# Kernel optimization log

Hardware: AMD Instinct MI355X
Metric: run time of the kernel (lower is better)

## Reference

```python
import jax, jax.numpy as jnp
import numpy as np

N_NODES = 50000
N_EDGES = 500000
D_IN, D_HID = 128, 256


def _add_self_loops(edge_index, n):
    loop = jnp.arange(n, dtype=edge_index.dtype)
    src = jnp.concatenate([edge_index[0], loop])
    dst = jnp.concatenate([edge_index[1], loop])
    return src, dst


def _gcn_layer(x, W, b, src, dst, dinv_sqrt, n):
    # x: [N, d_in] -> h: [N, d_out]
    h = x @ W
    # symmetric normalization D^{-1/2} (A+I) D^{-1/2}
    norm = dinv_sqrt[src] * dinv_sqrt[dst]          # [E+N]
    msg = h[src] * norm[:, None]                    # gather + scale
    agg = jax.ops.segment_sum(msg, dst, num_segments=n)  # scatter-add
    return agg + b


def setup_inputs() -> dict:
    key = jax.random.key(0)
    ks = jax.random.split(key, 8)
    x = jax.random.normal(ks[0], (N_NODES, D_IN), dtype=jnp.float32)
    edge_index = jax.random.randint(ks[1], (2, N_EDGES), 0, N_NODES, dtype=jnp.int64 if jax.config.read('jax_enable_x64') else jnp.int32)
    s = lambda fan_in: 1.0 / np.sqrt(fan_in)
    W1 = jax.random.uniform(ks[2], (D_IN, D_HID), jnp.float32, -s(D_IN), s(D_IN))
    b1 = jnp.zeros((D_HID,), jnp.float32)
    W2 = jax.random.uniform(ks[3], (D_HID, D_HID), jnp.float32, -s(D_HID), s(D_HID))
    b2 = jnp.zeros((D_HID,), jnp.float32)
    W3 = jax.random.uniform(ks[4], (D_HID, D_HID), jnp.float32, -s(D_HID), s(D_HID))
    b3 = jnp.zeros((D_HID,), jnp.float32)
    return {"x": x, "edge_index": edge_index, "W1": W1, "b1": b1,
            "W2": W2, "b2": b2, "W3": W3, "b3": b3}


def reference(x, edge_index, W1, b1, W2, b2, W3, b3):
    n = x.shape[0]
    src, dst = _add_self_loops(edge_index, n)
    # degree includes self loops (edge weight 1), as in torch_geometric GCNConv
    deg = jax.ops.segment_sum(jnp.ones_like(dst, dtype=x.dtype), dst, num_segments=n)
    dinv_sqrt = jnp.where(deg > 0, jax.lax.rsqrt(jnp.maximum(deg, 1e-12)), 0.0)
    h = jax.nn.relu(_gcn_layer(x, W1, b1, src, dst, dinv_sqrt, n))
    h = jax.nn.relu(_gcn_layer(h, W2, b2, src, dst, dinv_sqrt, n))
    h = _gcn_layer(h, W3, b3, src, dst, dinv_sqrt, n)
    return h
```

## Files before the change

### kernel.cpp

```cpp
#include <hip/hip_runtime.h>

#define NNODES 50000
#define NEDGES 500000
#define DIN 128
#define DHID 256
#define MPAD 50048
#define NI4 12500
#define NSB 49

typedef unsigned short u16;
typedef __attribute__((ext_vector_type(8))) _Float16 half8;
typedef __attribute__((ext_vector_type(4))) float f32x4;

__device__ __forceinline__ u16 f2h(float f) {
  union { _Float16 h; u16 u; } v; v.h = (_Float16)f; return v.u;
}
__device__ __forceinline__ float h2f(unsigned int u) {
  union { _Float16 h; u16 u; } v; v.u = (u16)u; return (float)v.h;
}

#define GLDS16(g, l) __builtin_amdgcn_global_load_lds( \
    (const __attribute__((address_space(1))) void*)(g), \
    (__attribute__((address_space(3))) void*)(l), 16, 0, 0)

__global__ void k_zero_i32(int* __restrict__ p, int n) {
  int i = blockIdx.x * blockDim.x + threadIdx.x;
  if (i < n) p[i] = 0;
}

__global__ void k_hist(const int* __restrict__ dst, int* __restrict__ deg, int e) {
  int i = blockIdx.x * blockDim.x + threadIdx.x;
  if (i < e) atomicAdd(&deg[dst[i]], 1);
}

__global__ __launch_bounds__(256) void k_blocksum(const int* __restrict__ deg,
                                                  int* __restrict__ partials) {
  __shared__ int red[256];
  int tid = threadIdx.x;
  int t4 = blockIdx.x * 256 + tid;
  int sum = 0;
  if (t4 < NI4) {
    int4 v = ((const int4*)deg)[t4];
    sum = v.x + v.y + v.z + v.w;
  }
  red[tid] = sum;
  __syncthreads();
  for (int off = 128; off > 0; off >>= 1) {
    if (tid < off) red[tid] += red[tid + off];
    __syncthreads();
  }
  if (tid == 0) partials[blockIdx.x] = red[0];
}

__global__ __launch_bounds__(256) void k_scan2(int* __restrict__ deg,
                                               const int* __restrict__ partials,
                                               int* __restrict__ row_ptr,
                                               float* __restrict__ dinv) {
  __shared__ int sdata[256];
  __shared__ int sprefix;
  int tid = threadIdx.x, bid = blockIdx.x;
  int t4 = bid * 256 + tid;
  int4 v = make_int4(0, 0, 0, 0);
  if (t4 < NI4) v = ((const int4*)deg)[t4];
  int tsum = v.x + v.y + v.z + v.w;
  sdata[tid] = tsum;
  if (tid == 0) {
    int pre = 0;
    for (int b = 0; b < bid; ++b) pre += partials[b];
    sprefix = pre;
  }
  __syncthreads();
  for (int off = 1; off < 256; off <<= 1) {
    int val = (tid >= off) ? sdata[tid - off] : 0;
    __syncthreads();
    sdata[tid] += val;
    __syncthreads();
  }
  if (t4 < NI4) {
    int run = sdata[tid] - tsum + sprefix;
    int base = t4 * 4;
    float4 dv;
    dv.x = rsqrtf((float)v.x + 1.0f);
    dv.y = rsqrtf((float)v.y + 1.0f);
    dv.z = rsqrtf((float)v.z + 1.0f);
    dv.w = rsqrtf((float)v.w + 1.0f);
    *(float4*)(dinv + base) = dv;
    row_ptr[base + 0] = run; run += v.x;
    row_ptr[base + 1] = run; run += v.y;
    row_ptr[base + 2] = run; run += v.z;
    row_ptr[base + 3] = run; run += v.w;
    if (base + 4 == NNODES) row_ptr[NNODES] = run;
    ((int4*)deg)[t4] = make_int4(0, 0, 0, 0);
  }
}

__global__ void k_fill(const int* __restrict__ src, const int* __restrict__ dst,
                       const float* __restrict__ dinv, const int* __restrict__ row_ptr,
                       int* __restrict__ cursor, int* __restrict__ csr_src,
                       float* __restrict__ csr_nrm, int e) {
  int i = blockIdx.x * blockDim.x + threadIdx.x;
  if (i < e) {
    int d = dst[i], s = src[i];
    int pos = row_ptr[d] + atomicAdd(&cursor[d], 1);
    csr_src[pos] = s;
    csr_nrm[pos] = dinv[s] * dinv[d];
  }
}

__global__ void k_x2f16(const float* __restrict__ x, u16* __restrict__ xh, int total4) {
  int i = blockIdx.x * blockDim.x + threadIdx.x;
  if (i >= total4) return;
  float4 v = ((const float4*)x)[i];
  ushort4 o;
  o.x = f2h(v.x); o.y = f2h(v.y); o.z = f2h(v.z); o.w = f2h(v.w);
  ((ushort4*)xh)[i] = o;
}

__global__ void k_splitW3(const float* __restrict__ W1f, u16* __restrict__ P1,
                          const float* __restrict__ W2f, u16* __restrict__ P2,
                          const float* __restrict__ W3f, u16* __restrict__ P3) {
  int i = blockIdx.x * blockDim.x + threadIdx.x;
  const int s1 = DIN * 256, s2 = s1 + DHID * 256, s3 = s2 + DHID * 256;
  if (i >= s3) return;
  const float* W; u16* P; int li;
  if (i < s1)      { W = W1f; P = P1; li = i; }
  else if (i < s2) { W = W2f; P = P2; li = i - s1; }
  else             { W = W3f; P = P3; li = i - s2; }
  int k = li >> 8, n = li & 255;
  int t = k >> 5, q = (k >> 3) & 3, j = k & 7;
  int c = n >> 4, m = n & 15;
  int f = (c * 64 + q * 16 + m) * 8 + j;
  float w = W[li] * 256.0f;
  u16 hi = f2h(w);
  u16 lo = f2h(w - h2f(hi));
  P[(size_t)t * 16384 + f] = hi;
  P[(size_t)t * 16384 + 8192 + f] = lo;
}

template<int W>
__global__ __launch_bounds__(256) void k_aggN(const u16* __restrict__ hf,
                                              const float* __restrict__ dinv,
                                              const int* __restrict__ row_ptr,
                                              const int* __restrict__ csr_src,
                                              const float* __restrict__ csr_nrm,
                                              u16* __restrict__ aout, int n) {
  constexpr int GL = W / 8;
  constexpr int NG = 64 / GL;
  const int lane = threadIdx.x & 63;
  const int wave = threadIdx.x >> 6;
  const int g = lane / GL;
  const int sub = lane % GL;
  const int coff = sub * 8;

  const int base = (blockIdx.x * 4 + wave) * NG + g;
  const int stride = gridDim.x * 4 * NG;

  for (int node = base; node < n; node += stride) {
    float acc[8];
    float di = dinv[node];
    float s2 = di * di;

    {
      half8 v = *(const half8*)(hf + (size_t)node * W + coff);
#pragma unroll
      for (int j = 0; j < 8; ++j) acc[j] = s2 * (float)v[j];
    }

    const int p0 = row_ptr[node];
    const int p1 = row_ptr[node + 1];
    for (int e = p0; e < p1; e += 4) {
      int i1 = e + 1 < p1 ? e + 1 : e;
      int i2 = e + 2 < p1 ? e + 2 : e;
      int i3 = e + 3 < p1 ? e + 3 : e;
      int s0i = csr_src[e], s1i = csr_src[i1], s2i = csr_src[i2], s3i = csr_src[i3];
      float w0 = csr_nrm[e];
      float w1 = e + 1 < p1 ? csr_nrm[i1] : 0.0f;
      float w2 = e + 2 < p1 ? csr_nrm[i2] : 0.0f;
      float w3 = e + 3 < p1 ? csr_nrm[i3] : 0.0f;
      half8 v0 = *(const half8*)(hf + (size_t)s0i * W + coff);
      half8 v1 = *(const half8*)(hf + (size_t)s1i * W + coff);
      half8 v2 = *(const half8*)(hf + (size_t)s2i * W + coff);
      half8 v3 = *(const half8*)(hf + (size_t)s3i * W + coff);
#pragma unroll
      for (int j = 0; j < 8; ++j) {
        acc[j] = fmaf(w0, (float)v0[j], acc[j]);
        acc[j] = fmaf(w1, (float)v1[j], acc[j]);
        acc[j] = fmaf(w2, (float)v2[j], acc[j]);
        acc[j] = fmaf(w3, (float)v3[j], acc[j]);
      }
    }

    uint4 o;
    o.x = (unsigned)f2h(acc[0]) | ((unsigned)f2h(acc[1]) << 16);
    o.y = (unsigned)f2h(acc[2]) | ((unsigned)f2h(acc[3]) << 16);
    o.z = (unsigned)f2h(acc[4]) | ((unsigned)f2h(acc[5]) << 16);
    o.w = (unsigned)f2h(acc[6]) | ((unsigned)f2h(acc[7]) << 16);
    *(uint4*)(aout + (size_t)node * W + coff) = o;
  }
}

template<int K, int EPI>
__global__ __launch_bounds__(256, 4) void k_gemm_mfma(const u16* __restrict__ A,
                                                      const u16* __restrict__ Bpk,
                                                      const float* __restrict__ bias,
                                                      u16* __restrict__ hf16,
                                                      float* __restrict__ outf) {
  __shared__ __align__(16) u16 Bs[16384];
  const int lane = threadIdx.x & 63;
  const int wave = threadIdx.x >> 6;
  const int rw = wave & 1, cw = wave >> 1;
  const int m0 = blockIdx.x * 64 + rw * 32;

  f32x4 acc0[8], acc1[8];
#pragma unroll
  for (int c = 0; c < 8; ++c) {
    acc0[c] = {0.f, 0.f, 0.f, 0.f};
    acc1[c] = {0.f, 0.f, 0.f, 0.f};
  }

  const u16* a0p = A + (size_t)(m0 + (lane & 15)) * K + ((lane >> 4) * 8);
  const u16* a1p = a0p + (size_t)16 * K;

  for (int t = 0; t < K / 32; ++t) {
    __syncthreads();
    {
      const char* gsrc = (const char*)(Bpk + (size_t)t * 16384);
      char* lbase = (char*)Bs;
#pragma unroll
      for (int it = 0; it < 8; ++it) {
        int off = (wave * 8 + it) * 1024 + lane * 16;
        GLDS16(gsrc + off, lbase + off);
      }
    }
    __syncthreads();

    half8 a0 = *(const half8*)(a0p + t * 32);
    half8 a1 = *(const half8*)(a1p + t * 32);
#pragma unroll
    for (int c = 0; c < 8; ++c) {
      const u16* fb = Bs + ((cw * 8 + c) * 64 + lane) * 8;
      half8 bh = *(const half8*)fb;
      half8 bl = *(const half8*)(fb + 8192);
      acc0[c] = __builtin_amdgcn_mfma_f32_16x16x32_f16(a0, bh, acc0[c], 0, 0, 0);
      acc0[c] = __builtin_amdgcn_mfma_f32_16x16x32_f16(a0, bl, acc0[c], 0, 0, 0);
      acc1[c] = __builtin_amdgcn_mfma_f32_16x16x32_f16(a1, bh, acc1[c], 0, 0, 0);
      acc1[c] = __builtin_amdgcn_mfma_f32_16x16x32_f16(a1, bl, acc1[c], 0, 0, 0);
    }
  }

  const int cbase = lane & 15;
  const int r0 = m0 + ((lane >> 4) * 4);
  const float sc = 1.0f / 256.0f;
#pragma unroll
  for (int c = 0; c < 8; ++c) {
    int col = (cw * 8 + c) * 16 + cbase;
    float bv = bias[col];
#pragma unroll
    for (int r = 0; r < 4; ++r) {
      float v0 = fmaf(acc0[c][r], sc, bv);
      float v1 = fmaf(acc1[c][r], sc, bv);
      if (EPI == 0) {
        v0 = fmaxf(v0, 0.f);
        v1 = fmaxf(v1, 0.f);
        hf16[(size_t)(r0 + r) * 256 + col] = f2h(v0);
        hf16[(size_t)(r0 + 16 + r) * 256 + col] = f2h(v1);
      } else {
        if (r0 + r < NNODES) outf[(size_t)(r0 + r) * 256 + col] = v0;
        if (r0 + 16 + r < NNODES) outf[(size_t)(r0 + 16 + r) * 256 + col] = v1;
      }
    }
  }
}

extern "C" void kernel_launch(void* const* d_in, const int* in_sizes, int n_in,
                              void* d_out, int out_size, void* d_ws, size_t ws_size,
                              hipStream_t stream) {
  const float* x  = (const float*)d_in[0];
  const int*   ei = (const int*)d_in[1];
  const float* W1 = (const float*)d_in[2];
  const float* b1 = (const float*)d_in[3];
  const float* W2 = (const float*)d_in[4];
  const float* b2 = (const float*)d_in[5];
  const float* W3 = (const float*)d_in[6];
  const float* b3 = (const float*)d_in[7];
  float* out = (float*)d_out;
  (void)in_sizes; (void)n_in; (void)out_size; (void)ws_size;

  char* ws = (char*)d_ws;
  size_t off = 0;
  auto alloc = [&](size_t bytes) -> void* {
    void* p = (void*)(ws + off);
    off += (bytes + 255) & ~(size_t)255;
    return p;
  };
  float* dinv    = (float*)alloc((size_t)NNODES * 4);
  int*   deg     = (int*)alloc((size_t)NNODES * 4);
  int*   row_ptr = (int*)alloc((size_t)(NNODES + 1) * 4);
  int*   partials= (int*)alloc((size_t)NSB * 4);
  int*   csr_src = (int*)alloc((size_t)NEDGES * 4);
  float* csr_nrm = (float*)alloc((size_t)NEDGES * 4);
  u16*   xh      = (u16*)alloc((size_t)NNODES * DIN * 2);
  u16*   hbuf    = (u16*)alloc((size_t)MPAD * 256 * 2);
  u16*   A1      = (u16*)alloc((size_t)MPAD * DIN * 2);
  u16*   A2      = (u16*)alloc((size_t)MPAD * 256 * 2);
  u16*   W1pk    = (u16*)alloc((size_t)(DIN / 32) * 16384 * 2);
  u16*   W2pk    = (u16*)alloc((size_t)(DHID / 32) * 16384 * 2);
  u16*   W3pk    = (u16*)alloc((size_t)(DHID / 32) * 16384 * 2);

  const int* e_src = ei;
  const int* e_dst = ei + NEDGES;

  const int tb = 256;
  k_zero_i32<<<(NNODES + tb - 1) / tb, tb, 0, stream>>>(deg, NNODES);
  k_hist<<<(NEDGES + tb - 1) / tb, tb, 0, stream>>>(e_dst, deg, NEDGES);
  k_blocksum<<<NSB, 256, 0, stream>>>(deg, partials);
  k_scan2<<<NSB, 256, 0, stream>>>(deg, partials, row_ptr, dinv);
  k_fill<<<(NEDGES + tb - 1) / tb, tb, 0, stream>>>(e_src, e_dst, dinv, row_ptr, deg,
                                                    csr_src, csr_nrm, NEDGES);

  int x4 = NNODES * DIN / 4;
  k_x2f16<<<(x4 + tb - 1) / tb, tb, 0, stream>>>(x, xh, x4);
  int wtot = (DIN + DHID + DHID) * 256;
  k_splitW3<<<(wtot + tb - 1) / tb, tb, 0, stream>>>(W1, W1pk, W2, W2pk, W3, W3pk);

  const int gblocks = MPAD / 64;
  const int aggrid = 2048;

  k_aggN<128><<<aggrid, 256, 0, stream>>>(xh, dinv, row_ptr, csr_src, csr_nrm,
                                          A1, NNODES);
  k_gemm_mfma<DIN, 0><<<gblocks, 256, 0, stream>>>(A1, W1pk, b1, hbuf, nullptr);
  k_aggN<256><<<aggrid, 256, 0, stream>>>(hbuf, dinv, row_ptr, csr_src, csr_nrm,
                                          A2, NNODES);
  k_gemm_mfma<DHID, 0><<<gblocks, 256, 0, stream>>>(A2, W2pk, b2, hbuf, nullptr);
  k_aggN<256><<<aggrid, 256, 0, stream>>>(hbuf, dinv, row_ptr, csr_src, csr_nrm,
                                          A2, NNODES);
  k_gemm_mfma<DHID, 1><<<gblocks, 256, 0, stream>>>(A2, W3pk, b3, nullptr, out);
}
```

Measured before the change: 337.3 us.

## Panelize GCN aggregation by feature columns and pack CSR src/norm into one word

Aggregation kernel now splits feature columns into 32-wide panels per block, with each block walking a contiguous chunk of nodes. Four lanes cover a node's panel and 16 nodes share a wave. The intent is better L2 locality, since each block touches only a narrow column slice of the gathered feature matrix. CSR source index and normalization weight are packed into one 64-bit word and read with nontemporal loads, and the edge loop is unrolled by 2 instead of 4. The trade-off is fewer gathers in flight per lane and more redundant CSR reads, since every panel rereads the edge list.

Result: slower. 463.4 us (+37.4%).

```diff
diff --git a/kernel.cpp b/kernel.cpp
--- a/kernel.cpp
+++ b/kernel.cpp
@@ -96,14 +96,14 @@
 
 __global__ void k_fill(const int* __restrict__ src, const int* __restrict__ dst,
                        const float* __restrict__ dinv, const int* __restrict__ row_ptr,
-                       int* __restrict__ cursor, int* __restrict__ csr_src,
-                       float* __restrict__ csr_nrm, int e) {
+                       int* __restrict__ cursor, long long* __restrict__ csr_pk, int e) {
   int i = blockIdx.x * blockDim.x + threadIdx.x;
   if (i < e) {
     int d = dst[i], s = src[i];
     int pos = row_ptr[d] + atomicAdd(&cursor[d], 1);
-    csr_src[pos] = s;
-    csr_nrm[pos] = dinv[s] * dinv[d];
+    float nrm = dinv[s] * dinv[d];
+    csr_pk[pos] = (long long)(unsigned)s |
+                  ((long long)__float_as_int(nrm) << 32);
   }
 }
 
@@ -138,64 +138,65 @@
 }
 
 template<int W>
-__global__ __launch_bounds__(256) void k_aggN(const u16* __restrict__ hf,
+__global__ __launch_bounds__(256) void k_aggP(const u16* __restrict__ hf,
                                               const float* __restrict__ dinv,
                                               const int* __restrict__ row_ptr,
-                                              const int* __restrict__ csr_src,
-                                              const float* __restrict__ csr_nrm,
+                                              const long long* __restrict__ csr_pk,
                                               u16* __restrict__ aout, int n) {
-  constexpr int GL = W / 8;
-  constexpr int NG = 64 / GL;
+  constexpr int NPAN = W / 32;
+  constexpr int PSH = (NPAN == 8) ? 3 : 2;
+  const int panel = blockIdx.x & (NPAN - 1);
+  const int chunk = blockIdx.x >> PSH;
+  const int nchunks = gridDim.x >> PSH;
+  const int CH = (n + nchunks - 1) / nchunks;
+
   const int lane = threadIdx.x & 63;
   const int wave = threadIdx.x >> 6;
-  const int g = lane / GL;
-  const int sub = lane % GL;
-  const int coff = sub * 8;
-
-  const int base = (blockIdx.x * 4 + wave) * NG + g;
-  const int stride = gridDim.x * 4 * NG;
-
-  for (int node = base; node < n; node += stride) {
-    float acc[8];
+  const int g = lane >> 2;
+  const int sub = lane & 3;
+  const int pc = panel * 32 + sub * 8;
+
+  const int start = chunk * CH;
+  int end = start + CH; if (end > n) end = n;
+
+  for (int node = start + wave * 16 + g; node < end; node += 64) {
     float di = dinv[node];
     float s2 = di * di;
-
+    float acc[8];
     {
-      half8 v = *(const half8*)(hf + (size_t)node * W + coff);
+      half8 v = *(const half8*)(hf + (size_t)node * W + pc);
 #pragma unroll
       for (int j = 0; j < 8; ++j) acc[j] = s2 * (float)v[j];
     }
-
     const int p0 = row_ptr[node];
     const int p1 = row_ptr[node + 1];
-    for (int e = p0; e < p1; e += 4) {
-      int i1 = e + 1 < p1 ? e + 1 : e;
-      int i2 = e + 2 < p1 ? e + 2 : e;
-      int i3 = e + 3 < p1 ? e + 3 : e;
-      int s0i = csr_src[e], s1i = csr_src[i1], s2i = csr_src[i2], s3i = csr_src[i3];
-      float w0 = csr_nrm[e];
-      float w1 = e + 1 < p1 ? csr_nrm[i1] : 0.0f;
-      float w2 = e + 2 < p1 ? csr_nrm[i2] : 0.0f;
-      float w3 = e + 3 < p1 ? csr_nrm[i3] : 0.0f;
-      half8 v0 = *(const half8*)(hf + (size_t)s0i * W + coff);
-      half8 v1 = *(const half8*)(hf + (size_t)s1i * W + coff);
-      half8 v2 = *(const half8*)(hf + (size_t)s2i * W + coff);
-      half8 v3 = *(const half8*)(hf + (size_t)s3i * W + coff);
+    int e = p0;
+    for (; e + 2 <= p1; e += 2) {
+      long long c0 = __builtin_nontemporal_load(csr_pk + e);
+      long long c1 = __builtin_nontemporal_load(csr_pk + e + 1);
+      int s0 = (int)c0;  float w0 = __int_as_float((int)(c0 >> 32));
+      int s1 = (int)c1;  float w1 = __int_as_float((int)(c1 >> 32));
+      half8 v0 = *(const half8*)(hf + (size_t)s0 * W + pc);
+      half8 v1 = *(const half8*)(hf + (size_t)s1 * W + pc);
 #pragma unroll
       for (int j = 0; j < 8; ++j) {
         acc[j] = fmaf(w0, (float)v0[j], acc[j]);
         acc[j] = fmaf(w1, (float)v1[j], acc[j]);
-        acc[j] = fmaf(w2, (float)v2[j], acc[j]);
-        acc[j] = fmaf(w3, (float)v3[j], acc[j]);
       }
     }
-
+    if (e < p1) {
+      long long c0 = __builtin_nontemporal_load(csr_pk + e);
+      int s0 = (int)c0;  float w0 = __int_as_float((int)(c0 >> 32));
+      half8 v0 = *(const half8*)(hf + (size_t)s0 * W + pc);
+#pragma unroll
+      for (int j = 0; j < 8; ++j) acc[j] = fmaf(w0, (float)v0[j], acc[j]);
+    }
     uint4 o;
     o.x = (unsigned)f2h(acc[0]) | ((unsigned)f2h(acc[1]) << 16);
     o.y = (unsigned)f2h(acc[2]) | ((unsigned)f2h(acc[3]) << 16);
     o.z = (unsigned)f2h(acc[4]) | ((unsigned)f2h(acc[5]) << 16);
     o.w = (unsigned)f2h(acc[6]) | ((unsigned)f2h(acc[7]) << 16);
-    *(uint4*)(aout + (size_t)node * W + coff) = o;
+    *(uint4*)(aout + (size_t)node * W + pc) = o;
   }
 }
 
@@ -297,8 +298,7 @@
   int*   deg     = (int*)alloc((size_t)NNODES * 4);
   int*   row_ptr = (int*)alloc((size_t)(NNODES + 1) * 4);
   int*   partials= (int*)alloc((size_t)NSB * 4);
-  int*   csr_src = (int*)alloc((size_t)NEDGES * 4);
-  float* csr_nrm = (float*)alloc((size_t)NEDGES * 4);
+  long long* csr_pk = (long long*)alloc((size_t)NEDGES * 8);
   u16*   xh      = (u16*)alloc((size_t)NNODES * DIN * 2);
   u16*   hbuf    = (u16*)alloc((size_t)MPAD * 256 * 2);
   u16*   A1      = (u16*)alloc((size_t)MPAD * DIN * 2);
@@ -316,7 +316,7 @@
   k_blocksum<<<NSB, 256, 0, stream>>>(deg, partials);
   k_scan2<<<NSB, 256, 0, stream>>>(deg, partials, row_ptr, dinv);
   k_fill<<<(NEDGES + tb - 1) / tb, tb, 0, stream>>>(e_src, e_dst, dinv, row_ptr, deg,
-                                                    csr_src, csr_nrm, NEDGES);
+                                                    csr_pk, NEDGES);
 
   int x4 = NNODES * DIN / 4;
   k_x2f16<<<(x4 + tb - 1) / tb, tb, 0, stream>>>(x, xh, x4);
@@ -326,13 +326,10 @@
   const int gblocks = MPAD / 64;
   const int aggrid = 2048;
 
-  k_aggN<128><<<aggrid, 256, 0, stream>>>(xh, dinv, row_ptr, csr_src, csr_nrm,
-                                          A1, NNODES);
+  k_aggP<128><<<aggrid, 256, 0, stream>>>(xh, dinv, row_ptr, csr_pk, A1, NNODES);
   k_gemm_mfma<DIN, 0><<<gblocks, 256, 0, stream>>>(A1, W1pk, b1, hbuf, nullptr);
-  k_aggN<256><<<aggrid, 256, 0, stream>>>(hbuf, dinv, row_ptr, csr_src, csr_nrm,
-                                          A2, NNODES);
+  k_aggP<256><<<aggrid, 256, 0, stream>>>(hbuf, dinv, row_ptr, csr_pk, A2, NNODES);
   k_gemm_mfma<DHID, 0><<<gblocks, 256, 0, stream>>>(A2, W2pk, b2, hbuf, nullptr);
-  k_aggN<256><<<aggrid, 256, 0, stream>>>(hbuf, dinv, row_ptr, csr_src, csr_nrm,
-                                          A2, NNODES);
+  k_aggP<256><<<aggrid, 256, 0, stream>>>(hbuf, dinv, row_ptr, csr_pk, A2, NNODES);
   k_gemm_mfma<DHID, 1><<<gblocks, 256, 0, stream>>>(A2, W3pk, b3, nullptr, out);
 }
```

## Fuse neighbor aggregation into MFMA GEMM via swizzled LDS A tile

Applied to the files above, without the earlier changes.

Merges the per-layer gather/aggregate kernel with the following GEMM. Each 64-row block first aggregates its nodes' neighbor features into an XOR-swizzled shared-memory A tile, then runs the MFMA GEMM straight from LDS. This drops the global round trip of the aggregated matrix and three kernel launches, and unrolls the edge loop to 8 gathers. In exchange, aggregation parallelism is tied to the GEMM grid (about 782 blocks), LDS use rises to as much as 64 KB per block, occupancy drops to launch_bounds 2, and gather latency is no longer overlapped across a persistent grid.

Result: slower. 351.2 us (+4.1%).

```diff
diff --git a/kernel.cpp b/kernel.cpp
--- a/kernel.cpp
+++ b/kernel.cpp
@@ -137,79 +137,81 @@
   P[(size_t)t * 16384 + 8192 + f] = lo;
 }
 
-template<int W>
-__global__ __launch_bounds__(256) void k_aggN(const u16* __restrict__ hf,
-                                              const float* __restrict__ dinv,
-                                              const int* __restrict__ row_ptr,
-                                              const int* __restrict__ csr_src,
-                                              const float* __restrict__ csr_nrm,
-                                              u16* __restrict__ aout, int n) {
-  constexpr int GL = W / 8;
-  constexpr int NG = 64 / GL;
-  const int lane = threadIdx.x & 63;
-  const int wave = threadIdx.x >> 6;
-  const int g = lane / GL;
-  const int sub = lane % GL;
-  const int coff = sub * 8;
-
-  const int base = (blockIdx.x * 4 + wave) * NG + g;
-  const int stride = gridDim.x * 4 * NG;
-
-  for (int node = base; node < n; node += stride) {
-    float acc[8];
-    float di = dinv[node];
-    float s2 = di * di;
-
-    {
-      half8 v = *(const half8*)(hf + (size_t)node * W + coff);
-#pragma unroll
-      for (int j = 0; j < 8; ++j) acc[j] = s2 * (float)v[j];
+template<int K, int EPI>
+__global__ __launch_bounds__(256, 2) void k_fused(const u16* __restrict__ hf,
+                                                  const float* __restrict__ dinv,
+                                                  const int* __restrict__ row_ptr,
+                                                  const int* __restrict__ csr_src,
+                                                  const float* __restrict__ csr_nrm,
+                                                  const u16* __restrict__ Bpk,
+                                                  const float* __restrict__ bias,
+                                                  u16* __restrict__ hf16,
+                                                  float* __restrict__ outf) {
+  __shared__ __align__(16) u16 As[64 * K];
+  __shared__ __align__(16) u16 Bs[16384];
+
+  {
+    constexpr int GL = K / 8;
+    constexpr int NGRP = 256 / GL;
+    constexpr int RPG = 64 / NGRP;
+    const int gg = threadIdx.x / GL;
+    const int sub = threadIdx.x % GL;
+    const int coff = sub * 8;
+    const int nbase = blockIdx.x * 64;
+
+    for (int k = 0; k < RPG; ++k) {
+      const int row = gg + k * NGRP;
+      const int node = nbase + row;
+      float acc[8];
+      if (node < NNODES) {
+        float di = dinv[node];
+        float s2 = di * di;
+        {
+          half8 v = *(const half8*)(hf + (size_t)node * K + coff);
+#pragma unroll
+          for (int j = 0; j < 8; ++j) acc[j] = s2 * (float)v[j];
+        }
+        const int p0 = row_ptr[node];
+        const int p1 = row_ptr[node + 1];
+        for (int e = p0; e < p1; e += 8) {
+          int idx[8]; float w[8];
+#pragma unroll
+          for (int q = 0; q < 8; ++q) {
+            int ii = (e + q < p1) ? e + q : p1 - 1;
+            idx[q] = csr_src[ii];
+            w[q] = (e + q < p1) ? csr_nrm[ii] : 0.0f;
+          }
+          half8 v[8];
+#pragma unroll
+          for (int q = 0; q < 8; ++q)
+            v[q] = *(const half8*)(hf + (size_t)idx[q] * K + coff);
+#pragma unroll
+          for (int q = 0; q < 8; ++q)
+#pragma unroll
+            for (int j = 0; j < 8; ++j)
+              acc[j] = fmaf(w[q], (float)v[q][j], acc[j]);
+        }
+      } else {
+#pragma unroll
+        for (int j = 0; j < 8; ++j) acc[j] = 0.0f;
+      }
+      const int wc = coff ^ ((row & 7) << 3);
+      uint4 o;
+      o.x = (unsigned)f2h(acc[0]) | ((unsigned)f2h(acc[1]) << 16);
+      o.y = (unsigned)f2h(acc[2]) | ((unsigned)f2h(acc[3]) << 16);
+      o.z = (unsigned)f2h(acc[4]) | ((unsigned)f2h(acc[5]) << 16);
+      o.w = (unsigned)f2h(acc[6]) | ((unsigned)f2h(acc[7]) << 16);
+      *(uint4*)&As[row * K + wc] = o;
     }
-
-    const int p0 = row_ptr[node];
-    const int p1 = row_ptr[node + 1];
-    for (int e = p0; e < p1; e += 4) {
-      int i1 = e + 1 < p1 ? e + 1 : e;
-      int i2 = e + 2 < p1 ? e + 2 : e;
-      int i3 = e + 3 < p1 ? e + 3 : e;
-      int s0i = csr_src[e], s1i = csr_src[i1], s2i = csr_src[i2], s3i = csr_src[i3];
-      float w0 = csr_nrm[e];
-      float w1 = e + 1 < p1 ? csr_nrm[i1] : 0.0f;
-      float w2 = e + 2 < p1 ? csr_nrm[i2] : 0.0f;
-      float w3 = e + 3 < p1 ? csr_nrm[i3] : 0.0f;
-      half8 v0 = *(const half8*)(hf + (size_t)s0i * W + coff);
-      half8 v1 = *(const half8*)(hf + (size_t)s1i * W + coff);
-      half8 v2 = *(const half8*)(hf + (size_t)s2i * W + coff);
-      half8 v3 = *(const half8*)(hf + (size_t)s3i * W + coff);
-#pragma unroll
-      for (int j = 0; j < 8; ++j) {
-        acc[j] = fmaf(w0, (float)v0[j], acc[j]);
-        acc[j] = fmaf(w1, (float)v1[j], acc[j]);
-        acc[j] = fmaf(w2, (float)v2[j], acc[j]);
-        acc[j] = fmaf(w3, (float)v3[j], acc[j]);
-      }
-    }
-
-    uint4 o;
-    o.x = (unsigned)f2h(acc[0]) | ((unsigned)f2h(acc[1]) << 16);
-    o.y = (unsigned)f2h(acc[2]) | ((unsigned)f2h(acc[3]) << 16);
-    o.z = (unsigned)f2h(acc[4]) | ((unsigned)f2h(acc[5]) << 16);
-    o.w = (unsigned)f2h(acc[6]) | ((unsigned)f2h(acc[7]) << 16);
-    *(uint4*)(aout + (size_t)node * W + coff) = o;
-  }
-}
-
-template<int K, int EPI>
-__global__ __launch_bounds__(256, 4) void k_gemm_mfma(const u16* __restrict__ A,
-                                                      const u16* __restrict__ Bpk,
-                                                      const float* __restrict__ bias,
-                                                      u16* __restrict__ hf16,
-                                                      float* __restrict__ outf) {
-  __shared__ __align__(16) u16 Bs[16384];
+  }
+
   const int lane = threadIdx.x & 63;
   const int wave = threadIdx.x >> 6;
   const int rw = wave & 1, cw = wave >> 1;
   const int m0 = blockIdx.x * 64 + rw * 32;
+  const int lr0 = rw * 32 + (lane & 15);
+  const int lr1 = lr0 + 16;
+  const int acoff = (lane >> 4) * 8;
 
   f32x4 acc0[8], acc1[8];
 #pragma unroll
@@ -217,9 +219,6 @@
     acc0[c] = {0.f, 0.f, 0.f, 0.f};
     acc1[c] = {0.f, 0.f, 0.f, 0.f};
   }
-
-  const u16* a0p = A + (size_t)(m0 + (lane & 15)) * K + ((lane >> 4) * 8);
-  const u16* a1p = a0p + (size_t)16 * K;
 
   for (int t = 0; t < K / 32; ++t) {
     __syncthreads();
@@ -234,8 +233,9 @@
     }
     __syncthreads();
 
-    half8 a0 = *(const half8*)(a0p + t * 32);
-    half8 a1 = *(const half8*)(a1p + t * 32);
+    const int ac = acoff + t * 32;
+    half8 a0 = *(const half8*)&As[lr0 * K + (ac ^ ((lr0 & 7) << 3))];
+    half8 a1 = *(const half8*)&As[lr1 * K + (ac ^ ((lr1 & 7) << 3))];
 #pragma unroll
     for (int c = 0; c < 8; ++c) {
       const u16* fb = Bs + ((cw * 8 + c) * 64 + lane) * 8;
@@ -300,9 +300,8 @@
   int*   csr_src = (int*)alloc((size_t)NEDGES * 4);
   float* csr_nrm = (float*)alloc((size_t)NEDGES * 4);
   u16*   xh      = (u16*)alloc((size_t)NNODES * DIN * 2);
-  u16*   hbuf    = (u16*)alloc((size_t)MPAD * 256 * 2);
-  u16*   A1      = (u16*)alloc((size_t)MPAD * DIN * 2);
-  u16*   A2      = (u16*)alloc((size_t)MPAD * 256 * 2);
+  u16*   hbufA   = (u16*)alloc((size_t)MPAD * 256 * 2);
+  u16*   hbufB   = (u16*)alloc((size_t)MPAD * 256 * 2);
   u16*   W1pk    = (u16*)alloc((size_t)(DIN / 32) * 16384 * 2);
   u16*   W2pk    = (u16*)alloc((size_t)(DHID / 32) * 16384 * 2);
   u16*   W3pk    = (u16*)alloc((size_t)(DHID / 32) * 16384 * 2);
@@ -324,15 +323,11 @@
   k_splitW3<<<(wtot + tb - 1) / tb, tb, 0, stream>>>(W1, W1pk, W2, W2pk, W3, W3pk);
 
   const int gblocks = MPAD / 64;
-  const int aggrid = 2048;
-
-  k_aggN<128><<<aggrid, 256, 0, stream>>>(xh, dinv, row_ptr, csr_src, csr_nrm,
-                                          A1, NNODES);
-  k_gemm_mfma<DIN, 0><<<gblocks, 256, 0, stream>>>(A1, W1pk, b1, hbuf, nullptr);
-  k_aggN<256><<<aggrid, 256, 0, stream>>>(hbuf, dinv, row_ptr, csr_src, csr_nrm,
-                                          A2, NNODES);
-  k_gemm_mfma<DHID, 0><<<gblocks, 256, 0, stream>>>(A2, W2pk, b2, hbuf, nullptr);
-  k_aggN<256><<<aggrid, 256, 0, stream>>>(hbuf, dinv, row_ptr, csr_src, csr_nrm,
-                                          A2, NNODES);
-  k_gemm_mfma<DHID, 1><<<gblocks, 256, 0, stream>>>(A2, W3pk, b3, nullptr, out);
-}
+
+  k_fused<DIN, 0><<<gblocks, 256, 0, stream>>>(xh, dinv, row_ptr, csr_src, csr_nrm,
+                                               W1pk, b1, hbufA, nullptr);
+  k_fused<DHID, 0><<<gblocks, 256, 0, stream>>>(hbufA, dinv, row_ptr, csr_src, csr_nrm,
+                                                W2pk, b2, hbufB, nullptr);
+  k_fused<DHID, 1><<<gblocks, 256, 0, stream>>>(hbufB, dinv, row_ptr, csr_src, csr_nrm,
+                                                W3pk, b3, nullptr, out);
+}
```

## Panelize feature matrix by column and assign panels to XCDs with dynamic chunk queues

Applied to the files above, without the earlier changes.

Node features are stored in 32-column panels (panel-major layout), and the aggregation kernel hands each block whole chunks of nodes for one panel. Blocks take work from per-panel atomic queues that start at the panel matching their XCD id. The aim is to keep each panel's working set inside one XCD's L2 and so cut cross-XCD gather traffic. The zeroing, x conversion and weight packing kernels are merged into one prep kernel, and the two hidden-feature buffers are separated. The costs are 4-lane groups issuing narrower per-row gathers, atomic scheduling overhead, and the assumption that XCD ids map cleanly onto the panel count.

Result: slower. 660.4 us (+95.8%).

```diff
diff --git a/kernel.cpp b/kernel.cpp
--- a/kernel.cpp
+++ b/kernel.cpp
@@ -7,6 +7,8 @@
 #define MPAD 50048
 #define NI4 12500
 #define NSB 49
+#define CH 200
+#define NCHUNK 250
 
 typedef unsigned short u16;
 typedef __attribute__((ext_vector_type(8))) _Float16 half8;
@@ -19,14 +21,15 @@
   union { _Float16 h; u16 u; } v; v.u = (u16)u; return (float)v.h;
 }
 
+__device__ __forceinline__ int get_xcd() {
+  int x;
+  asm volatile("s_getreg_b32 %0, hwreg(HW_REG_XCC_ID)" : "=s"(x));
+  return x;
+}
+
 #define GLDS16(g, l) __builtin_amdgcn_global_load_lds( \
     (const __attribute__((address_space(1))) void*)(g), \
     (__attribute__((address_space(3))) void*)(l), 16, 0, 0)
-
-__global__ void k_zero_i32(int* __restrict__ p, int n) {
-  int i = blockIdx.x * blockDim.x + threadIdx.x;
-  if (i < n) p[i] = 0;
-}
 
 __global__ void k_hist(const int* __restrict__ dst, int* __restrict__ deg, int e) {
   int i = blockIdx.x * blockDim.x + threadIdx.x;
@@ -107,95 +110,117 @@
   }
 }
 
-__global__ void k_x2f16(const float* __restrict__ x, u16* __restrict__ xh, int total4) {
+__global__ void k_prep(const float* __restrict__ x, u16* __restrict__ xh, int total4,
+                       int* __restrict__ deg, int* __restrict__ q,
+                       const float* __restrict__ W1f, u16* __restrict__ P1,
+                       const float* __restrict__ W2f, u16* __restrict__ P2,
+                       const float* __restrict__ W3f, u16* __restrict__ P3) {
   int i = blockIdx.x * blockDim.x + threadIdx.x;
-  if (i >= total4) return;
-  float4 v = ((const float4*)x)[i];
-  ushort4 o;
-  o.x = f2h(v.x); o.y = f2h(v.y); o.z = f2h(v.z); o.w = f2h(v.w);
-  ((ushort4*)xh)[i] = o;
-}
-
-__global__ void k_splitW3(const float* __restrict__ W1f, u16* __restrict__ P1,
-                          const float* __restrict__ W2f, u16* __restrict__ P2,
-                          const float* __restrict__ W3f, u16* __restrict__ P3) {
-  int i = blockIdx.x * blockDim.x + threadIdx.x;
+  if (i < 24) q[i] = 0;
+  if (i < NI4) ((int4*)deg)[i] = make_int4(0, 0, 0, 0);
+  if (i < total4) {
+    float4 v = ((const float4*)x)[i];
+    ushort4 o;
+    o.x = f2h(v.x); o.y = f2h(v.y); o.z = f2h(v.z); o.w = f2h(v.w);
+    int node = i >> 5;
+    int col = (i & 31) * 4;
+    int pan = col >> 5, wi = col & 31;
+    *(ushort4*)(xh + ((size_t)pan * MPAD + node) * 32 + wi) = o;
+  }
   const int s1 = DIN * 256, s2 = s1 + DHID * 256, s3 = s2 + DHID * 256;
-  if (i >= s3) return;
-  const float* W; u16* P; int li;
-  if (i < s1)      { W = W1f; P = P1; li = i; }
-  else if (i < s2) { W = W2f; P = P2; li = i - s1; }
-  else             { W = W3f; P = P3; li = i - s2; }
-  int k = li >> 8, n = li & 255;
-  int t = k >> 5, q = (k >> 3) & 3, j = k & 7;
-  int c = n >> 4, m = n & 15;
-  int f = (c * 64 + q * 16 + m) * 8 + j;
-  float w = W[li] * 256.0f;
-  u16 hi = f2h(w);
-  u16 lo = f2h(w - h2f(hi));
-  P[(size_t)t * 16384 + f] = hi;
-  P[(size_t)t * 16384 + 8192 + f] = lo;
-}
-
-template<int W>
-__global__ __launch_bounds__(256) void k_aggN(const u16* __restrict__ hf,
+  if (i < s3) {
+    const float* W; u16* P; int li;
+    if (i < s1)      { W = W1f; P = P1; li = i; }
+    else if (i < s2) { W = W2f; P = P2; li = i - s1; }
+    else             { W = W3f; P = P3; li = i - s2; }
+    int k = li >> 8, n = li & 255;
+    int t = k >> 5, qq = (k >> 3) & 3, j = k & 7;
+    int c = n >> 4, m = n & 15;
+    int f = (c * 64 + qq * 16 + m) * 8 + j;
+    float w = W[li] * 256.0f;
+    u16 hi = f2h(w);
+    u16 lo = f2h(w - h2f(hi));
+    P[(size_t)t * 16384 + f] = hi;
+    P[(size_t)t * 16384 + 8192 + f] = lo;
+  }
+}
+
+template<int K>
+__global__ __launch_bounds__(256) void k_aggX(const u16* __restrict__ hp,
                                               const float* __restrict__ dinv,
                                               const int* __restrict__ row_ptr,
                                               const int* __restrict__ csr_src,
                                               const float* __restrict__ csr_nrm,
+                                              int* __restrict__ q,
                                               u16* __restrict__ aout, int n) {
-  constexpr int GL = W / 8;
-  constexpr int NG = 64 / GL;
+  constexpr int NPAN = K / 32;
+  __shared__ int sh_pan, sh_chunk, sh_next;
   const int lane = threadIdx.x & 63;
-  const int wave = threadIdx.x >> 6;
-  const int g = lane / GL;
-  const int sub = lane % GL;
-  const int coff = sub * 8;
-
-  const int base = (blockIdx.x * 4 + wave) * NG + g;
-  const int stride = gridDim.x * 4 * NG;
-
-  for (int node = base; node < n; node += stride) {
-    float acc[8];
-    float di = dinv[node];
-    float s2 = di * di;
-
-    {
-      half8 v = *(const half8*)(hf + (size_t)node * W + coff);
-#pragma unroll
-      for (int j = 0; j < 8; ++j) acc[j] = s2 * (float)v[j];
-    }
-
-    const int p0 = row_ptr[node];
-    const int p1 = row_ptr[node + 1];
-    for (int e = p0; e < p1; e += 4) {
-      int i1 = e + 1 < p1 ? e + 1 : e;
-      int i2 = e + 2 < p1 ? e + 2 : e;
-      int i3 = e + 3 < p1 ? e + 3 : e;
-      int s0i = csr_src[e], s1i = csr_src[i1], s2i = csr_src[i2], s3i = csr_src[i3];
-      float w0 = csr_nrm[e];
-      float w1 = e + 1 < p1 ? csr_nrm[i1] : 0.0f;
-      float w2 = e + 2 < p1 ? csr_nrm[i2] : 0.0f;
-      float w3 = e + 3 < p1 ? csr_nrm[i3] : 0.0f;
-      half8 v0 = *(const half8*)(hf + (size_t)s0i * W + coff);
-      half8 v1 = *(const half8*)(hf + (size_t)s1i * W + coff);
-      half8 v2 = *(const half8*)(hf + (size_t)s2i * W + coff);
-      half8 v3 = *(const half8*)(hf + (size_t)s3i * W + coff);
-#pragma unroll
-      for (int j = 0; j < 8; ++j) {
-        acc[j] = fmaf(w0, (float)v0[j], acc[j]);
-        acc[j] = fmaf(w1, (float)v1[j], acc[j]);
-        acc[j] = fmaf(w2, (float)v2[j], acc[j]);
-        acc[j] = fmaf(w3, (float)v3[j], acc[j]);
-      }
-    }
-
-    uint4 o;
-    o.x = (unsigned)f2h(acc[0]) | ((unsigned)f2h(acc[1]) << 16);
-    o.y = (unsigned)f2h(acc[2]) | ((unsigned)f2h(acc[3]) << 16);
-    o.z = (unsigned)f2h(acc[4]) | ((unsigned)f2h(acc[5]) << 16);
-    o.w = (unsigned)f2h(acc[6]) | ((unsigned)f2h(acc[7]) << 16);
-    *(uint4*)(aout + (size_t)node * W + coff) = o;
+  const int sub = lane & 3;
+  const int gbase = lane & ~3;
+
+  const int xcd = get_xcd() & (NPAN - 1);
+
+  for (;;) {
+    __syncthreads();
+    if (threadIdx.x == 0) {
+      int found = -1, fc = 0;
+      for (int off = 0; off < NPAN; ++off) {
+        int p = (xcd + off) & (NPAN - 1);
+        int c = atomicAdd(&q[p], 1);
+        if (c < NCHUNK) { found = p; fc = c; break; }
+      }
+      sh_pan = found; sh_chunk = fc; sh_next = 0;
+    }
+    __syncthreads();
+    const int pan = sh_pan;
+    if (pan < 0) break;
+    const int nb = sh_chunk * CH;
+    const int nend = (nb + CH < n) ? nb + CH : n;
+    const u16* hbase = hp + (size_t)pan * MPAD * 32 + sub * 8;
+
+    for (;;) {
+      int r = 0;
+      if (sub == 0) r = atomicAdd(&sh_next, 1);
+      r = __shfl(r, gbase);
+      const int node = nb + r;
+      if (node >= nend) break;
+
+      float di = dinv[node];
+      float s2 = di * di;
+      float acc[8];
+      {
+        half8 v = *(const half8*)(hbase + (size_t)node * 32);
+#pragma unroll
+        for (int j = 0; j < 8; ++j) acc[j] = s2 * (float)v[j];
+      }
+      const int p0 = row_ptr[node];
+      const int p1 = row_ptr[node + 1];
+      for (int e = p0; e < p1; e += 4) {
+        int idx[4]; float w[4];
+#pragma unroll
+        for (int t = 0; t < 4; ++t) {
+          int ii = (e + t < p1) ? e + t : p1 - 1;
+          idx[t] = __builtin_nontemporal_load(csr_src + ii);
+          w[t] = (e + t < p1) ? __builtin_nontemporal_load(csr_nrm + ii) : 0.0f;
+        }
+        half8 v[4];
+#pragma unroll
+        for (int t = 0; t < 4; ++t)
+          v[t] = *(const half8*)(hbase + (size_t)idx[t] * 32);
+#pragma unroll
+        for (int t = 0; t < 4; ++t)
+#pragma unroll
+          for (int j = 0; j < 8; ++j)
+            acc[j] = fmaf(w[t], (float)v[t][j], acc[j]);
+      }
+      uint4 o;
+      o.x = (unsigned)f2h(acc[0]) | ((unsigned)f2h(acc[1]) << 16);
+      o.y = (unsigned)f2h(acc[2]) | ((unsigned)f2h(acc[3]) << 16);
+      o.z = (unsigned)f2h(acc[4]) | ((unsigned)f2h(acc[5]) << 16);
+      o.w = (unsigned)f2h(acc[6]) | ((unsigned)f2h(acc[7]) << 16);
+      *(uint4*)(aout + (size_t)node * K + pan * 32 + sub * 8) = o;
+    }
   }
 }
 
@@ -255,6 +280,7 @@
   for (int c = 0; c < 8; ++c) {
     int col = (cw * 8 + c) * 16 + cbase;
     float bv = bias[col];
+    const size_t pbase = ((size_t)(col >> 5) * MPAD) * 32 + (col & 31);
 #pragma unroll
     for (int r = 0; r < 4; ++r) {
       float v0 = fmaf(acc0[c][r], sc, bv);
@@ -262,8 +288,8 @@
       if (EPI == 0) {
         v0 = fmaxf(v0, 0.f);
         v1 = fmaxf(v1, 0.f);
-        hf16[(size_t)(r0 + r) * 256 + col] = f2h(v0);
-        hf16[(size_t)(r0 + 16 + r) * 256 + col] = f2h(v1);
+        hf16[pbase + (size_t)(r0 + r) * 32] = f2h(v0);
+        hf16[pbase + (size_t)(r0 + 16 + r) * 32] = f2h(v1);
       } else {
         if (r0 + r < NNODES) outf[(size_t)(r0 + r) * 256 + col] = v0;
         if (r0 + 16 + r < NNODES) outf[(size_t)(r0 + 16 + r) * 256 + col] = v1;
@@ -297,10 +323,12 @@
   int*   deg     = (int*)alloc((size_t)NNODES * 4);
   int*   row_ptr = (int*)alloc((size_t)(NNODES + 1) * 4);
   int*   partials= (int*)alloc((size_t)NSB * 4);
+  int*   qzs     = (int*)alloc((size_t)24 * 4);
   int*   csr_src = (int*)alloc((size_t)NEDGES * 4);
   float* csr_nrm = (float*)alloc((size_t)NEDGES * 4);
-  u16*   xh      = (u16*)alloc((size_t)NNODES * DIN * 2);
-  u16*   hbuf    = (u16*)alloc((size_t)MPAD * 256 * 2);
+  u16*   xh      = (u16*)alloc((size_t)MPAD * DIN * 2);
+  u16*   hbufA   = (u16*)alloc((size_t)MPAD * 256 * 2);
+  u16*   hbufB   = (u16*)alloc((size_t)MPAD * 256 * 2);
   u16*   A1      = (u16*)alloc((size_t)MPAD * DIN * 2);
   u16*   A2      = (u16*)alloc((size_t)MPAD * 256 * 2);
   u16*   W1pk    = (u16*)alloc((size_t)(DIN / 32) * 16384 * 2);
@@ -311,28 +339,25 @@
   const int* e_dst = ei + NEDGES;
 
   const int tb = 256;
-  k_zero_i32<<<(NNODES + tb - 1) / tb, tb, 0, stream>>>(deg, NNODES);
+  int x4 = NNODES * DIN / 4;
+  k_prep<<<(x4 + tb - 1) / tb, tb, 0, stream>>>(x, xh, x4, deg, qzs,
+                                                W1, W1pk, W2, W2pk, W3, W3pk);
   k_hist<<<(NEDGES + tb - 1) / tb, tb, 0, stream>>>(e_dst, deg, NEDGES);
   k_blocksum<<<NSB, 256, 0, stream>>>(deg, partials);
   k_scan2<<<NSB, 256, 0, stream>>>(deg, partials, row_ptr, dinv);
   k_fill<<<(NEDGES + tb - 1) / tb, tb, 0, stream>>>(e_src, e_dst, dinv, row_ptr, deg,
                                                     csr_src, csr_nrm, NEDGES);
 
-  int x4 = NNODES * DIN / 4;
-  k_x2f16<<<(x4 + tb - 1) / tb, tb, 0, stream>>>(x, xh, x4);
-  int wtot = (DIN + DHID + DHID) * 256;
-  k_splitW3<<<(wtot + tb - 1) / tb, tb, 0, stream>>>(W1, W1pk, W2, W2pk, W3, W3pk);
-
   const int gblocks = MPAD / 64;
-  const int aggrid = 2048;
-
-  k_aggN<128><<<aggrid, 256, 0, stream>>>(xh, dinv, row_ptr, csr_src, csr_nrm,
-                                          A1, NNODES);
-  k_gemm_mfma<DIN, 0><<<gblocks, 256, 0, stream>>>(A1, W1pk, b1, hbuf, nullptr);
-  k_aggN<256><<<aggrid, 256, 0, stream>>>(hbuf, dinv, row_ptr, csr_src, csr_nrm,
-                                          A2, NNODES);
-  k_gemm_mfma<DHID, 0><<<gblocks, 256, 0, stream>>>(A2, W2pk, b2, hbuf, nullptr);
-  k_aggN<256><<<aggrid, 256, 0, stream>>>(hbuf, dinv, row_ptr, csr_src, csr_nrm,
-                                          A2, NNODES);
+  const int ablocks = 1024;
+
+  k_aggX<DIN><<<ablocks, 256, 0, stream>>>(xh, dinv, row_ptr, csr_src, csr_nrm,
+                                           qzs + 0, A1, NNODES);
+  k_gemm_mfma<DIN, 0><<<gblocks, 256, 0, stream>>>(A1, W1pk, b1, hbufA, nullptr);
+  k_aggX<DHID><<<ablocks, 256, 0, stream>>>(hbufA, dinv, row_ptr, csr_src, csr_nrm,
+                                            qzs + 8, A2, NNODES);
+  k_gemm_mfma<DHID, 0><<<gblocks, 256, 0, stream>>>(A2, W2pk, b2, hbufB, nullptr);
+  k_aggX<DHID><<<ablocks, 256, 0, stream>>>(hbufB, dinv, row_ptr, csr_src, csr_nrm,
+                                            qzs + 16, A2, NNODES);
   k_gemm_mfma<DHID, 1><<<gblocks, 256, 0, stream>>>(A2, W3pk, b3, nullptr, out);
 }
```
